# Kernel optimization log

Hardware: AMD Instinct MI355X
Metric: run time of the kernel (lower is better)

## Reference

```python
import jax, jax.numpy as jnp
import numpy as np

N = 50_000      # num_nodes
E = 1_600_000   # num_edges
R = 8           # num_relations
D = 128         # hidden_dim
L = 3           # num_layers
EPS = 1e-5


def setup_inputs() -> dict:
    key = jax.random.key(0)
    ks = jax.random.split(key, 10)
    x = jnp.arange(N, dtype=jnp.int64) if jax.config.jax_enable_x64 else jnp.arange(N, dtype=jnp.int32)
    edge_index = jax.random.randint(ks[0], (2, E), 0, N)
    edge_type = jax.random.randint(ks[1], (E,), 0, R)
    emb = jax.random.normal(ks[2], (N, D), dtype=jnp.float32) * (1.0 / np.sqrt(D))
    w_rel = jax.random.normal(ks[3], (L, R, D, D), dtype=jnp.float32) * (1.0 / np.sqrt(D))
    w_root = jax.random.normal(ks[4], (L, D, D), dtype=jnp.float32) * (1.0 / np.sqrt(D))
    bias = jax.random.normal(ks[5], (L, D), dtype=jnp.float32) * 0.01
    gamma = 1.0 + 0.1 * jax.random.normal(ks[6], (L, D), dtype=jnp.float32)
    beta = 0.1 * jax.random.normal(ks[7], (L, D), dtype=jnp.float32)
    return {"x": x, "edge_index": edge_index, "edge_type": edge_type,
            "emb": emb, "w_rel": w_rel, "w_root": w_root, "bias": bias,
            "gamma": gamma, "beta": beta}


def _layer_norm(h, g, b):
    mu = jnp.mean(h, axis=-1, keepdims=True)
    var = jnp.mean(jnp.square(h - mu), axis=-1, keepdims=True)
    return (h - mu) * jax.lax.rsqrt(var + EPS) * g + b


def _rgcn_conv(h, src, dst, etype, w_rel, w_root, b):
    # PyG RGCNConv: per-relation mean aggregation of transformed neighbors + root transform + bias
    hr = jnp.einsum('nd,rdf->rnf', h, w_rel)          # [R, N, D] relation-transformed features
    msg = hr[etype, src]                               # [E, D] gather per edge
    seg = etype * N + dst                              # combined (relation, target) segment id
    sums = jax.ops.segment_sum(msg, seg, num_segments=R * N)            # [R*N, D]
    cnt = jax.ops.segment_sum(jnp.ones((msg.shape[0],), h.dtype), seg, num_segments=R * N)
    mean = sums / jnp.maximum(cnt, 1.0)[:, None]
    agg = mean.reshape(R, N, D).sum(axis=0)            # sum over relations
    return agg + h @ w_root + b


def reference(x, edge_index, edge_type, emb, w_rel, w_root, bias, gamma, beta):
    src, dst = edge_index[0], edge_index[1]
    h = emb[x]                                         # node embedding lookup
    for i in range(L):
        h_new = _rgcn_conv(h, src, dst, edge_type, w_rel[i], w_root[i], bias[i])
        h_new = jax.nn.relu(_layer_norm(h_new, gamma[i], beta[i]))
        # dropout is identity in eval/reference mode
        h = h + h_new if i > 0 else h_new
    return h
```

## Files before the change

### kernel.cpp

```cpp
#include <hip/hip_runtime.h>

#define NN 50000
#define NE 1600000
#define NR 8
#define ND 128
#define NL 3
#define RN (NR * NN)
#define LN_EPS 1e-5f
#define PADF 132

#define NBKT 196
#define BSH 11
#define STRIDE_PB 10240
#define BIN_BLOCKS 1000
#define EPB 1600
#define I4PB 400
#define MM_BLOCKS_SA ((NN + 127) / 128)
#define MM_BLOCKS_FU ((NN + 63) / 64)

#define PREP_G (NN * 64)
#define PREP_W (27 * 16384)
#define PREP_TOT (PREP_G + PREP_W)
#define PREP_BLOCKS ((PREP_TOT + 255) / 256)

#define WS_H    0
#define WS_ROW  14400000
#define WS_BCUR 16000064
#define WS_ADJ  16004096
#define WS_WB   22404096
#define WS_BIG  23288832
#define WS_NEED_NEW (23288832ULL + 9ULL * NN * 256)

typedef __attribute__((ext_vector_type(8))) short short8;
typedef __attribute__((ext_vector_type(4))) float float4v;
typedef __attribute__((ext_vector_type(4))) unsigned uint4v;

__device__ __forceinline__ float bflo(unsigned u) { return __uint_as_float(u << 16); }
__device__ __forceinline__ float bfhi(unsigned u) { return __uint_as_float(u & 0xFFFF0000u); }
__device__ __forceinline__ unsigned f2bf(float f) {
    unsigned u = __float_as_uint(f);
    return (u + 0x7FFFu + ((u >> 16) & 1u)) >> 16;
}
__device__ __forceinline__ unsigned pack2(float lo, float hi) {
    return f2bf(lo) | (f2bf(hi) << 16);
}

__global__ __launch_bounds__(256) void k_prepbin(const int* __restrict__ x,
                                                 const float* __restrict__ emb,
                                                 const float* __restrict__ w_rel,
                                                 const float* __restrict__ w_root,
                                                 const int* __restrict__ src,
                                                 const int* __restrict__ dst,
                                                 const int* __restrict__ et,
                                                 unsigned* __restrict__ h,
                                                 unsigned short* __restrict__ wb,
                                                 int* __restrict__ bcur,
                                                 unsigned* __restrict__ stage) {
    __shared__ int lcnt[256];
    __shared__ int loff[256];
    __shared__ int lcur[256];
    __shared__ int sbase[256];
    __shared__ int tmp[256];
    __shared__ unsigned srt[EPB];
    __shared__ unsigned char bkt[EPB];

    int tid = threadIdx.x;
    if (blockIdx.x >= BIN_BLOCKS) {
        int i = (blockIdx.x - BIN_BLOCKS) * 256 + tid;
        if (i < PREP_G) {
            int n = i >> 6, dw = i & 63;
            float2 v = *(const float2*)&emb[(size_t)x[n] * ND + 2 * dw];
            h[i] = pack2(v.x, v.y);
            return;
        }
        i -= PREP_G;
        if (i < PREP_W) {
            int m = i >> 14;
            int idx = i & 16383;
            int j = idx & 7;
            int lane = (idx >> 3) & 63;
            int ft = (idx >> 9) & 7;
            int kk = idx >> 12;
            int row = kk * 32 + (lane >> 4) * 8 + j;
            int col = ft * 16 + (lane & 15);
            const float* W = (m < 24) ? (w_rel + (size_t)m * 16384)
                                      : (w_root + (size_t)(m - 24) * 16384);
            wb[i] = (unsigned short)f2bf(W[row * ND + col]);
        }
        return;
    }

    lcnt[tid] = 0;
    __syncthreads();

    int base4 = blockIdx.x * I4PB;
    const int4* s4p = (const int4*)src;
    const int4* d4p = (const int4*)dst;
    const int4* t4p = (const int4*)et;

    for (int i4 = tid; i4 < I4PB; i4 += 256) {
        int4 d4 = d4p[base4 + i4];
        int4 t4 = t4p[base4 + i4];
        atomicAdd(&lcnt[(t4.x * NN + d4.x) >> BSH], 1);
        atomicAdd(&lcnt[(t4.y * NN + d4.y) >> BSH], 1);
        atomicAdd(&lcnt[(t4.z * NN + d4.z) >> BSH], 1);
        atomicAdd(&lcnt[(t4.w * NN + d4.w) >> BSH], 1);
    }
    __syncthreads();
    int own = lcnt[tid];
    tmp[tid] = own;
    __syncthreads();
    for (int off = 1; off < 256; off <<= 1) {
        int v = (tid >= off) ? tmp[tid - off] : 0;
        __syncthreads();
        tmp[tid] += v;
        __syncthreads();
    }
    int excl = tmp[tid] - own;
    loff[tid] = excl;
    lcur[tid] = excl;
    if (tid < NBKT) sbase[tid] = atomicAdd(&bcur[tid], own);
    __syncthreads();

    for (int i4 = tid; i4 < I4PB; i4 += 256) {
        int4 s4 = s4p[base4 + i4];
        int4 d4 = d4p[base4 + i4];
        int4 t4 = t4p[base4 + i4];
        int segs[4] = {t4.x * NN + d4.x, t4.y * NN + d4.y,
                       t4.z * NN + d4.z, t4.w * NN + d4.w};
        int srcs[4] = {s4.x, s4.y, s4.z, s4.w};
#pragma unroll
        for (int j = 0; j < 4; j++) {
            int seg = segs[j];
            int b = seg >> BSH;
            unsigned rec = ((unsigned)(seg & 2047) << 16) | (unsigned)srcs[j];
            int pos = atomicAdd(&lcur[b], 1);
            srt[pos] = rec;
            bkt[pos] = (unsigned char)b;
        }
    }
    __syncthreads();
    for (int i = tid; i < EPB; i += 256) {
        int b = bkt[i];
        int idx = sbase[b] + (i - loff[b]);
        if (idx < STRIDE_PB)
            stage[(size_t)b * STRIDE_PB + idx] = srt[i];
    }
}

__device__ __forceinline__ void binB_body(const unsigned* __restrict__ stage,
                                          const int* __restrict__ bcur,
                                          int* __restrict__ rowstart,
                                          int* __restrict__ adj,
                                          int b, int tid,
                                          int* tmp, int* lcnt2, int* loff2,
                                          unsigned short* srt2, int* misc) {
    int bv = (tid < NBKT) ? bcur[tid] : 0;
    tmp[tid] = bv;
    __syncthreads();
    for (int off = 1; off < 256; off <<= 1) {
        int v = (tid >= off) ? tmp[tid - off] : 0;
        __syncthreads();
        tmp[tid] += v;
        __syncthreads();
    }
    if (tid == b) { misc[0] = tmp[tid] - bv; misc[1] = bv; }
    for (int j = tid; j < 2048; j += 256) lcnt2[j] = 0;
    __syncthreads();

    int n = misc[1];
    n = n < STRIDE_PB ? n : STRIDE_PB;
    const unsigned* sp = stage + (size_t)b * STRIDE_PB;
    for (int i = tid; i < n; i += 256)
        atomicAdd(&lcnt2[sp[i] >> 16], 1);
    __syncthreads();

    int v8[8];
    int s8 = 0;
    int base8 = tid * 8;
#pragma unroll
    for (int j = 0; j < 8; j++) { v8[j] = lcnt2[base8 + j]; s8 += v8[j]; }
    tmp[tid] = s8;
    __syncthreads();
    for (int off = 1; off < 256; off <<= 1) {
        int v = (tid >= off) ? tmp[tid - off] : 0;
        __syncthreads();
        tmp[tid] += v;
        __syncthreads();
    }
    int run = tmp[tid] - s8;
#pragma unroll
    for (int j = 0; j < 8; j++) { loff2[base8 + j] = run; run += v8[j]; }
    __syncthreads();
    for (int j = tid; j < 2048; j += 256) lcnt2[j] = loff2[j];
    __syncthreads();

    for (int i = tid; i < n; i += 256) {
        unsigned rec = sp[i];
        int pos = atomicAdd(&lcnt2[rec >> 16], 1);
        srt2[pos] = (unsigned short)(rec & 0xFFFFu);
    }
    __syncthreads();

    int gb = misc[0];
    for (int i = tid; i < n; i += 256) adj[gb + i] = (int)srt2[i];
    int segbase = b << BSH;
    for (int j = tid; j < 2048; j += 256) {
        int seg = segbase + j;
        if (seg < RN) rowstart[seg] = gb + loff2[j];
    }
    if (b == NBKT - 1 && tid == 0) rowstart[RN] = NE;
}

typedef unsigned TRarr[16][66];

template <int NG>
__device__ __forceinline__ void mm_body(const unsigned* __restrict__ h32,
                                        const unsigned short* __restrict__ wrel,
                                        const unsigned short* __restrict__ wroot,
                                        unsigned* __restrict__ hr,
                                        int mb, int tid,
                                        uint4* SB4, TRarr* TRp) {
    const unsigned short* SBs = (const unsigned short*)SB4;
    int wave = tid >> 6, lane = tid & 63;
    int quad = lane >> 4, l15 = lane & 15;
    int pr = l15 & 1;

    int rbase[NG];
    short8 af[NG][4];
#pragma unroll
    for (int g = 0; g < NG; g++) {
        rbase[g] = mb * (64 * NG) + g * 64 + wave * 16;
        int gi = rbase[g] + l15; gi = gi < NN ? gi : NN - 1;
        const unsigned* H = h32 + (size_t)gi * 64;
#pragma unroll
        for (int kk = 0; kk < 4; kk++)
            af[g][kk] = *(const short8*)&H[kk * 16 + quad * 4];
    }

    for (int m = 0; m < 9; m++) {
        const unsigned short* W = (m < 8) ? (wrel + (size_t)m * 16384) : wroot;
        __syncthreads();
        {
            const uint4* Wg = (const uint4*)W;
#pragma unroll
            for (int i = 0; i < 8; i++) SB4[tid + 256 * i] = Wg[tid + 256 * i];
        }
        __syncthreads();

        float4v ac[NG][8];
#pragma unroll
        for (int g = 0; g < NG; g++)
#pragma unroll
            for (int i = 0; i < 8; i++) ac[g][i] = (float4v){0.f, 0.f, 0.f, 0.f};
#pragma unroll
        for (int kk = 0; kk < 4; kk++) {
#pragma unroll
            for (int ft = 0; ft < 8; ft++) {
                short8 bf = *(const short8*)&SBs[((kk * 8 + ft) * 64 + lane) * 8];
#pragma unroll
                for (int g = 0; g < NG; g++)
                    ac[g][ft] = __builtin_amdgcn_mfma_f32_16x16x32_bf16(af[g][kk], bf, ac[g][ft], 0, 0, 0);
            }
        }

        unsigned* hrm = hr + (size_t)m * NN * 64;
#pragma unroll
        for (int g = 0; g < NG; g++) {
#pragma unroll
            for (int ft = 0; ft < 8; ft++) {
                float4v part;
#pragma unroll
                for (int rg = 0; rg < 4; rg++) part[rg] = __shfl_xor(ac[g][ft][rg], 1, 64);
                if ((ft & 1) == pr) {
                    int a = l15 >> 1;
#pragma unroll
                    for (int rg = 0; rg < 4; rg++) {
                        float lo = pr ? part[rg] : ac[g][ft][rg];
                        float hi = pr ? ac[g][ft][rg] : part[rg];
                        TRp[wave][quad * 4 + rg][ft * 8 + a] = pack2(lo, hi);
                    }
                }
            }
#pragma unroll
            for (int ps = 0; ps < 4; ps++) {
                int ri = ps * 4 + quad;
                uint4 v = *(const uint4*)&TRp[wave][ri][l15 * 4];
                int row = rbase[g] + ri;
                if (row < NN)
                    *(uint4*)&hrm[(size_t)row * 64 + l15 * 4] = v;
            }
        }
    }
}

__global__ __launch_bounds__(256) void k_binB_mm(const unsigned* __restrict__ stage,
                                                 const int* __restrict__ bcur,
                                                 int* __restrict__ rowstart,
                                                 int* __restrict__ adj,
                                                 const unsigned* __restrict__ h32,
                                                 const unsigned short* __restrict__ wrel,
                                                 const unsigned short* __restrict__ wroot,
                                                 unsigned* __restrict__ hr) {
    __shared__ uint4 SMEM[3104];
    int tid = threadIdx.x;
    if (blockIdx.x < NBKT) {
        int* tmp = (int*)SMEM;
        int* lcnt2 = (int*)SMEM + 256;
        int* loff2 = (int*)SMEM + 2304;
        unsigned short* srt2 = (unsigned short*)((int*)SMEM + 4352);
        int* misc = (int*)SMEM + 9472;
        binB_body(stage, bcur, rowstart, adj, blockIdx.x, tid,
                  tmp, lcnt2, loff2, srt2, misc);
    } else {
        mm_body<1>(h32, wrel, wroot, hr, blockIdx.x - NBKT, tid,
                   SMEM, (TRarr*)(SMEM + 2048));
    }
}

__global__ __launch_bounds__(256) void k_binB(const unsigned* __restrict__ stage,
                                              const int* __restrict__ bcur,
                                              int* __restrict__ rowstart,
                                              int* __restrict__ adj) {
    __shared__ uint4 SMEM[2369];
    int tid = threadIdx.x;
    int* tmp = (int*)SMEM;
    int* lcnt2 = (int*)SMEM + 256;
    int* loff2 = (int*)SMEM + 2304;
    unsigned short* srt2 = (unsigned short*)((int*)SMEM + 4352);
    int* misc = (int*)SMEM + 9472;
    binB_body(stage, bcur, rowstart, adj, blockIdx.x, tid,
              tmp, lcnt2, loff2, srt2, misc);
}

__global__ __launch_bounds__(256) void k_mm(const unsigned* __restrict__ h32,
                                            const unsigned short* __restrict__ wrel,
                                            const unsigned short* __restrict__ wroot,
                                            unsigned* __restrict__ hr) {
    __shared__ uint4 SMEM[3104];
    mm_body<2>(h32, wrel, wroot, hr, blockIdx.x, threadIdx.x,
               SMEM, (TRarr*)(SMEM + 2048));
}

#define AGA(u)                                  \
    a0 += bflo(u.x); a1 += bfhi(u.x);           \
    a2 += bflo(u.y); a3 += bfhi(u.y);           \
    a4 += bflo(u.z); a5 += bfhi(u.z);           \
    a6 += bflo(u.w); a7 += bfhi(u.w);
#define AGC(u)                                  \
    c0 += bflo(u.x); c1 += bfhi(u.x);           \
    c2 += bflo(u.y); c3 += bfhi(u.y);           \
    c4 += bflo(u.z); c5 += bfhi(u.z);           \
    c6 += bflo(u.w); c7 += bfhi(u.w);

__global__ __launch_bounds__(256) void k_aggln(const unsigned* __restrict__ hr,
                                               unsigned* __restrict__ h32,
                                               const int* __restrict__ adj,
                                               const int* __restrict__ rowstart,
                                               const float* __restrict__ bias,
                                               const float* __restrict__ gamma,
                                               const float* __restrict__ beta,
                                               float* __restrict__ out_f,
                                               int add_res, int last) {
    int n = (blockIdx.x * 256 + threadIdx.x) >> 4;
    int l15 = threadIdx.x & 15;

    float t0 = 0.f, t1 = 0.f, t2 = 0.f, t3 = 0.f,
          t4 = 0.f, t5 = 0.f, t6 = 0.f, t7 = 0.f;

    for (int r = 0; r < NR; r++) {
        int seg = r * NN + n;
        int st = rowstart[seg], en = rowstart[seg + 1];
        st = st < 0 ? 0 : st;
        en = en > NE ? NE : en;
        const unsigned* T = hr + (size_t)r * NN * 64;

        float a0 = 0.f, a1 = 0.f, a2 = 0.f, a3 = 0.f,
              a4 = 0.f, a5 = 0.f, a6 = 0.f, a7 = 0.f;
        float c0 = 0.f, c1 = 0.f, c2 = 0.f, c3 = 0.f,
              c4 = 0.f, c5 = 0.f, c6 = 0.f, c7 = 0.f;
        int p = st;
        for (; p + 3 < en; p += 4) {
            unsigned s0 = (unsigned)adj[p],     s1 = (unsigned)adj[p + 1];
            unsigned s2 = (unsigned)adj[p + 2], s3 = (unsigned)adj[p + 3];
            uint4 u0 = *(const uint4*)&T[(size_t)s0 * 64 + l15 * 4];
            uint4 u1 = *(const uint4*)&T[(size_t)s1 * 64 + l15 * 4];
            uint4 u2 = *(const uint4*)&T[(size_t)s2 * 64 + l15 * 4];
            uint4 u3 = *(const uint4*)&T[(size_t)s3 * 64 + l15 * 4];
            AGA(u0) AGC(u1) AGA(u2) AGC(u3)
        }
        for (; p + 1 < en; p += 2) {
            unsigned s0 = (unsigned)adj[p], s1 = (unsigned)adj[p + 1];
            uint4 u0 = *(const uint4*)&T[(size_t)s0 * 64 + l15 * 4];
            uint4 u1 = *(const uint4*)&T[(size_t)s1 * 64 + l15 * 4];
            AGA(u0) AGC(u1)
        }
        if (p < en) {
            unsigned s0 = (unsigned)adj[p];
            uint4 u0 = *(const uint4*)&T[(size_t)s0 * 64 + l15 * 4];
            AGA(u0)
        }
        int d = en - st;
        float sc = 1.0f / (float)(d > 1 ? d : 1);
        t0 += (a0 + c0) * sc; t1 += (a1 + c1) * sc;
        t2 += (a2 + c2) * sc; t3 += (a3 + c3) * sc;
        t4 += (a4 + c4) * sc; t5 += (a5 + c5) * sc;
        t6 += (a6 + c6) * sc; t7 += (a7 + c7) * sc;
    }

    {
        uint4 u = *(const uint4*)&hr[((size_t)8 * NN + n) * 64 + l15 * 4];
        t0 += bflo(u.x); t1 += bfhi(u.x);
        t2 += bflo(u.y); t3 += bfhi(u.y);
        t4 += bflo(u.z); t5 += bfhi(u.z);
        t6 += bflo(u.w); t7 += bfhi(u.w);
    }
    int f0 = 8 * l15;
    {
        float4 b0 = *(const float4*)&bias[f0];
        float4 b1 = *(const float4*)&bias[f0 + 4];
        t0 += b0.x; t1 += b0.y; t2 += b0.z; t3 += b0.w;
        t4 += b1.x; t5 += b1.y; t6 += b1.z; t7 += b1.w;
    }

    float s = t0 + t1 + t2 + t3 + t4 + t5 + t6 + t7;
#pragma unroll
    for (int off = 1; off < 16; off <<= 1) s += __shfl_xor(s, off, 64);
    float mu = s * (1.0f / ND);
    float e0 = t0 - mu, e1 = t1 - mu, e2 = t2 - mu, e3 = t3 - mu,
          e4 = t4 - mu, e5 = t5 - mu, e6 = t6 - mu, e7 = t7 - mu;
    float vs = e0 * e0 + e1 * e1 + e2 * e2 + e3 * e3 +
               e4 * e4 + e5 * e5 + e6 * e6 + e7 * e7;
#pragma unroll
    for (int off = 1; off < 16; off <<= 1) vs += __shfl_xor(vs, off, 64);
    float rr = rsqrtf(vs * (1.0f / ND) + LN_EPS);

    float4 g0 = *(const float4*)&gamma[f0];
    float4 g1 = *(const float4*)&gamma[f0 + 4];
    float4 be0 = *(const float4*)&beta[f0];
    float4 be1 = *(const float4*)&beta[f0 + 4];
    float o0 = fmaxf(e0 * rr * g0.x + be0.x, 0.0f);
    float o1 = fmaxf(e1 * rr * g0.y + be0.y, 0.0f);
    float o2 = fmaxf(e2 * rr * g0.z + be0.z, 0.0f);
    float o3 = fmaxf(e3 * rr * g0.w + be0.w, 0.0f);
    float o4 = fmaxf(e4 * rr * g1.x + be1.x, 0.0f);
    float o5 = fmaxf(e5 * rr * g1.y + be1.y, 0.0f);
    float o6 = fmaxf(e6 * rr * g1.z + be1.z, 0.0f);
    float o7 = fmaxf(e7 * rr * g1.w + be1.w, 0.0f);

    if (add_res) {
        uint4 u = *(const uint4*)&h32[(size_t)n * 64 + l15 * 4];
        o0 += bflo(u.x); o1 += bfhi(u.x);
        o2 += bflo(u.y); o3 += bfhi(u.y);
        o4 += bflo(u.z); o5 += bfhi(u.z);
        o6 += bflo(u.w); o7 += bfhi(u.w);
    }
    if (last) {
        *(float4*)&out_f[(size_t)n * ND + f0] = make_float4(o0, o1, o2, o3);
        *(float4*)&out_f[(size_t)n * ND + f0 + 4] = make_float4(o4, o5, o6, o7);
    } else {
        uint4 w;
        w.x = pack2(o0, o1); w.y = pack2(o2, o3);
        w.z = pack2(o4, o5); w.w = pack2(o6, o7);
        *(uint4*)&h32[(size_t)n * 64 + l15 * 4] = w;
    }
}


__global__ __launch_bounds__(256) void k_agg(const unsigned* __restrict__ h32,
                                             const int* __restrict__ adj,
                                             const int* __restrict__ rowstart,
                                             unsigned* __restrict__ S) {
    int q = (blockIdx.x * 256 + threadIdx.x) >> 4;
    int l15 = threadIdx.x & 15;
    int r = q / NN;
    int n = q - r * NN;
    int st = rowstart[q], en = rowstart[q + 1];
    st = st < 0 ? 0 : st;
    en = en > NE ? NE : en;
    float a0 = 0.f, a1 = 0.f, a2 = 0.f, a3 = 0.f,
          a4 = 0.f, a5 = 0.f, a6 = 0.f, a7 = 0.f;
    float c0 = 0.f, c1 = 0.f, c2 = 0.f, c3 = 0.f,
          c4 = 0.f, c5 = 0.f, c6 = 0.f, c7 = 0.f;
    int p = st;
    for (; p + 3 < en; p += 4) {
        unsigned s0 = (unsigned)adj[p],     s1 = (unsigned)adj[p + 1];
        unsigned s2 = (unsigned)adj[p + 2], s3 = (unsigned)adj[p + 3];
        uint4 u0 = *(const uint4*)&h32[(size_t)s0 * 64 + l15 * 4];
        uint4 u1 = *(const uint4*)&h32[(size_t)s1 * 64 + l15 * 4];
        uint4 u2 = *(const uint4*)&h32[(size_t)s2 * 64 + l15 * 4];
        uint4 u3 = *(const uint4*)&h32[(size_t)s3 * 64 + l15 * 4];
        AGA(u0) AGC(u1) AGA(u2) AGC(u3)
    }
    for (; p < en; p++) {
        unsigned s0 = (unsigned)adj[p];
        uint4 u0 = *(const uint4*)&h32[(size_t)s0 * 64 + l15 * 4];
        AGA(u0)
    }
    int d = en - st;
    float sc = 1.0f / (float)(d > 1 ? d : 1);
    a0 = (a0 + c0) * sc; a1 = (a1 + c1) * sc;
    a2 = (a2 + c2) * sc; a3 = (a3 + c3) * sc;
    a4 = (a4 + c4) * sc; a5 = (a5 + c5) * sc;
    a6 = (a6 + c6) * sc; a7 = (a7 + c7) * sc;
    uint4v w;
    w.x = pack2(a0, a1); w.y = pack2(a2, a3);
    w.z = pack2(a4, a5); w.w = pack2(a6, a7);
    __builtin_nontemporal_store(w, (uint4v*)&S[(size_t)n * 512 + r * 64 + l15 * 4]);
}

__global__ __launch_bounds__(256) void k_gemm(const unsigned* __restrict__ S,
                                              unsigned* __restrict__ h32,
                                              const unsigned short* __restrict__ wrel,
                                              const unsigned short* __restrict__ wroot,
                                              const float* __restrict__ bias,
                                              const float* __restrict__ gamma,
                                              const float* __restrict__ beta,
                                              float* __restrict__ out_f,
                                              int add_res, int last) {
    __shared__ char smraw[4 * 16 * PADF * 4];
    float* SLF = (float*)smraw;
    uint4* SB4 = (uint4*)smraw;
    const unsigned short* SBs = (const unsigned short*)smraw;

    int tid = threadIdx.x;
    int wave = tid >> 6, lane = tid & 63;
    int quad = lane >> 4, l15 = lane & 15;
    int w0 = blockIdx.x * 64 + wave * 16;
    int gi = w0 + l15; gi = gi < NN ? gi : NN - 1;
    float* WF = SLF + wave * 16 * PADF;

    float4v acc[8];
#pragma unroll
    for (int i = 0; i < 8; i++) acc[i] = (float4v){0.f, 0.f, 0.f, 0.f};

    const unsigned* Sr = S + (size_t)gi * 512;
    for (int r = 0; r < NR; r++) {
        short8 afr[4];
#pragma unroll
        for (int kk = 0; kk < 4; kk++)
            afr[kk] = *(const short8*)&Sr[r * 64 + kk * 16 + quad * 4];
        __syncthreads();
        {
            const uint4* Wg = (const uint4*)(wrel + (size_t)r * 16384);
#pragma unroll
            for (int i = 0; i < 8; i++) SB4[tid + 256 * i] = Wg[tid + 256 * i];
        }
        __syncthreads();
#pragma unroll
        for (int kk = 0; kk < 4; kk++) {
#pragma unroll
            for (int ft = 0; ft < 8; ft++) {
                short8 bf = *(const short8*)&SBs[((kk * 8 + ft) * 64 + lane) * 8];
                acc[ft] = __builtin_amdgcn_mfma_f32_16x16x32_bf16(afr[kk], bf, acc[ft], 0, 0, 0);
            }
        }
    }
    {
        const unsigned* Hr = h32 + (size_t)gi * 64;
        short8 afr[4];
#pragma unroll
        for (int kk = 0; kk < 4; kk++)
            afr[kk] = *(const short8*)&Hr[kk * 16 + quad * 4];
        __syncthreads();
        {
            const uint4* Wg = (const uint4*)wroot;
#pragma unroll
            for (int i = 0; i < 8; i++) SB4[tid + 256 * i] = Wg[tid + 256 * i];
        }
        __syncthreads();
#pragma unroll
        for (int kk = 0; kk < 4; kk++) {
#pragma unroll
            for (int ft = 0; ft < 8; ft++) {
                short8 bf = *(const short8*)&SBs[((kk * 8 + ft) * 64 + lane) * 8];
                acc[ft] = __builtin_amdgcn_mfma_f32_16x16x32_bf16(afr[kk], bf, acc[ft], 0, 0, 0);
            }
        }
    }
    __syncthreads();

#pragma unroll
    for (int ft = 0; ft < 8; ft++)
#pragma unroll
        for (int rg = 0; rg < 4; rg++)
            WF[(quad * 4 + rg) * PADF + ft * 16 + l15] = acc[ft][rg];

    float2 bia = *(const float2*)&bias[2 * lane];
    float2 gam = *(const float2*)&gamma[2 * lane];
    float2 bet = *(const float2*)&beta[2 * lane];

    for (int i = 0; i < 16; i++) {
        int g = w0 + i;
        if (g >= NN) continue;
        float v0 = WF[i * PADF + 2 * lane] + bia.x;
        float v1 = WF[i * PADF + 2 * lane + 1] + bia.y;
        float s = v0 + v1;
#pragma unroll
        for (int off = 32; off > 0; off >>= 1) s += __shfl_xor(s, off, 64);
        float mu = s * (1.0f / ND);
        float e0 = v0 - mu, e1 = v1 - mu;
        float vs = e0 * e0 + e1 * e1;
#pragma unroll
        for (int off = 32; off > 0; off >>= 1) vs += __shfl_xor(vs, off, 64);
        float rr = rsqrtf(vs * (1.0f / ND) + LN_EPS);
        float o0 = fmaxf(e0 * rr * gam.x + bet.x, 0.0f);
        float o1 = fmaxf(e1 * rr * gam.y + bet.y, 0.0f);
        if (add_res) {
            unsigned u = h32[(size_t)g * 64 + lane];
            o0 += bflo(u);
            o1 += bfhi(u);
        }
        if (last) {
            *(float2*)&out_f[(size_t)g * ND + 2 * lane] = make_float2(o0, o1);
        } else {
            h32[(size_t)g * 64 + lane] = pack2(o0, o1);
        }
    }
}

extern "C" void kernel_launch(void* const* d_in, const int* in_sizes, int n_in,
                              void* d_out, int out_size, void* d_ws, size_t ws_size,
                              hipStream_t stream) {
    const int*   x      = (const int*)d_in[0];
    const int*   ei     = (const int*)d_in[1];
    const int*   et     = (const int*)d_in[2];
    const float* emb    = (const float*)d_in[3];
    const float* w_rel  = (const float*)d_in[4];
    const float* w_root = (const float*)d_in[5];
    const float* bias   = (const float*)d_in[6];
    const float* gamma  = (const float*)d_in[7];
    const float* beta   = (const float*)d_in[8];
    float* out = (float*)d_out;

    char* ws = (char*)d_ws;
    unsigned* h        = (unsigned*)(ws + WS_H);
    int*      rowstart = (int*)     (ws + WS_ROW);
    int*      bcur     = (int*)     (ws + WS_BCUR);
    int*      adj      = (int*)     (ws + WS_ADJ);
    unsigned short* wb = (unsigned short*)(ws + WS_WB);
    unsigned* big      = (unsigned*)(ws + WS_BIG);
    unsigned* stage    = (unsigned*)d_out;

    const int* src = ei;
    const int* dst = ei + NE;

    hipMemsetAsync(bcur, 0, NBKT * sizeof(int), stream);

    k_prepbin<<<BIN_BLOCKS + PREP_BLOCKS, 256, 0, stream>>>(
        x, emb, w_rel, w_root, src, dst, et, h, wb, bcur, stage);

    if (ws_size >= WS_NEED_NEW) {
        k_binB_mm<<<NBKT + MM_BLOCKS_FU, 256, 0, stream>>>(
            stage, bcur, rowstart, adj,
            h, wb, wb + (size_t)24 * 16384, big);
        k_aggln<<<NN * 16 / 256, 256, 0, stream>>>(
            big, h, adj, rowstart,
            bias, gamma, beta, out, 0, 0);
        for (int l = 1; l < NL; l++) {
            k_mm<<<MM_BLOCKS_SA, 256, 0, stream>>>(
                h, wb + (size_t)l * 8 * 16384, wb + (size_t)(24 + l) * 16384, big);
            k_aggln<<<NN * 16 / 256, 256, 0, stream>>>(
                big, h, adj, rowstart,
                bias + l * ND, gamma + l * ND, beta + l * ND,
                out, 1, l == NL - 1);
        }
    } else {
        k_binB<<<NBKT, 256, 0, stream>>>(stage, bcur, rowstart, adj);
        for (int l = 0; l < NL; l++) {
            k_agg<<<RN * 16 / 256, 256, 0, stream>>>(h, adj, rowstart, big);
            k_gemm<<<(NN + 63) / 64, 256, 0, stream>>>(
                big, h,
                wb + (size_t)l * 8 * 16384, wb + (size_t)(24 + l) * 16384,
                bias + l * ND, gamma + l * ND, beta + l * ND,
                out, l > 0, l == NL - 1);
        }
    }
}
```

Before: 499.2 us.

## Sort edges by destination node and pack relation and degree into adjacency entries

```diff
diff --git a/kernel.cpp b/kernel.cpp
--- a/kernel.cpp
+++ b/kernel.cpp
@@ -7,7 +7,6 @@
 #define NL 3
 #define RN (NR * NN)
 #define LN_EPS 1e-5f
-#define PADF 132
 
 #define NBKT 196
 #define BSH 11
@@ -24,16 +23,14 @@
 #define PREP_BLOCKS ((PREP_TOT + 255) / 256)
 
 #define WS_H    0
-#define WS_ROW  14400000
+#define WS_NS   14400000
 #define WS_BCUR 16000064
 #define WS_ADJ  16004096
 #define WS_WB   22404096
 #define WS_BIG  23288832
-#define WS_NEED_NEW (23288832ULL + 9ULL * NN * 256)
 
 typedef __attribute__((ext_vector_type(8))) short short8;
 typedef __attribute__((ext_vector_type(4))) float float4v;
-typedef __attribute__((ext_vector_type(4))) unsigned uint4v;
 
 __device__ __forceinline__ float bflo(unsigned u) { return __uint_as_float(u << 16); }
 __device__ __forceinline__ float bfhi(unsigned u) { return __uint_as_float(u & 0xFFFF0000u); }
@@ -101,10 +98,10 @@
     for (int i4 = tid; i4 < I4PB; i4 += 256) {
         int4 d4 = d4p[base4 + i4];
         int4 t4 = t4p[base4 + i4];
-        atomicAdd(&lcnt[(t4.x * NN + d4.x) >> BSH], 1);
-        atomicAdd(&lcnt[(t4.y * NN + d4.y) >> BSH], 1);
-        atomicAdd(&lcnt[(t4.z * NN + d4.z) >> BSH], 1);
-        atomicAdd(&lcnt[(t4.w * NN + d4.w) >> BSH], 1);
+        atomicAdd(&lcnt[(d4.x * 8 + t4.x) >> BSH], 1);
+        atomicAdd(&lcnt[(d4.y * 8 + t4.y) >> BSH], 1);
+        atomicAdd(&lcnt[(d4.z * 8 + t4.z) >> BSH], 1);
+        atomicAdd(&lcnt[(d4.w * 8 + t4.w) >> BSH], 1);
     }
     __syncthreads();
     int own = lcnt[tid];
@@ -126,14 +123,14 @@
         int4 s4 = s4p[base4 + i4];
         int4 d4 = d4p[base4 + i4];
         int4 t4 = t4p[base4 + i4];
-        int segs[4] = {t4.x * NN + d4.x, t4.y * NN + d4.y,
-                       t4.z * NN + d4.z, t4.w * NN + d4.w};
+        int keys[4] = {d4.x * 8 + t4.x, d4.y * 8 + t4.y,
+                       d4.z * 8 + t4.z, d4.w * 8 + t4.w};
         int srcs[4] = {s4.x, s4.y, s4.z, s4.w};
 #pragma unroll
         for (int j = 0; j < 4; j++) {
-            int seg = segs[j];
-            int b = seg >> BSH;
-            unsigned rec = ((unsigned)(seg & 2047) << 16) | (unsigned)srcs[j];
+            int key = keys[j];
+            int b = key >> BSH;
+            unsigned rec = ((unsigned)(key & 2047) << 16) | (unsigned)srcs[j];
             int pos = atomicAdd(&lcur[b], 1);
             srt[pos] = rec;
             bkt[pos] = (unsigned char)b;
@@ -150,8 +147,8 @@
 
 __device__ __forceinline__ void binB_body(const unsigned* __restrict__ stage,
                                           const int* __restrict__ bcur,
-                                          int* __restrict__ rowstart,
-                                          int* __restrict__ adj,
+                                          int* __restrict__ nodestart,
+                                          unsigned* __restrict__ adj,
                                           int b, int tid,
                                           int* tmp, int* lcnt2, int* loff2,
                                           unsigned short* srt2, int* misc) {
@@ -203,13 +200,19 @@
     __syncthreads();
 
     int gb = misc[0];
-    for (int i = tid; i < n; i += 256) adj[gb + i] = (int)srt2[i];
     int segbase = b << BSH;
-    for (int j = tid; j < 2048; j += 256) {
-        int seg = segbase + j;
-        if (seg < RN) rowstart[seg] = gb + loff2[j];
-    }
-    if (b == NBKT - 1 && tid == 0) rowstart[RN] = NE;
+#pragma unroll
+    for (int jj = 0; jj < 8; jj++) {
+        int j = base8 + jj;
+        int key = segbase + j;
+        if (key >= RN) break;
+        int s = loff2[j], e = lcnt2[j];
+        int d = e - s; d = d > 4095 ? 4095 : d;
+        unsigned tag = ((unsigned)(key & 7) << 28) | ((unsigned)d << 16);
+        for (int i = s; i < e; i++) adj[gb + i] = tag | (unsigned)srt2[i];
+        if ((key & 7) == 0) nodestart[key >> 3] = gb + s;
+    }
+    if (b == NBKT - 1 && tid == 0) nodestart[NN] = NE;
 }
 
 typedef unsigned TRarr[16][66];
@@ -296,8 +299,8 @@
 
 __global__ __launch_bounds__(256) void k_binB_mm(const unsigned* __restrict__ stage,
                                                  const int* __restrict__ bcur,
-                                                 int* __restrict__ rowstart,
-                                                 int* __restrict__ adj,
+                                                 int* __restrict__ nodestart,
+                                                 unsigned* __restrict__ adj,
                                                  const unsigned* __restrict__ h32,
                                                  const unsigned short* __restrict__ wrel,
                                                  const unsigned short* __restrict__ wroot,
@@ -310,27 +313,12 @@
         int* loff2 = (int*)SMEM + 2304;
         unsigned short* srt2 = (unsigned short*)((int*)SMEM + 4352);
         int* misc = (int*)SMEM + 9472;
-        binB_body(stage, bcur, rowstart, adj, blockIdx.x, tid,
+        binB_body(stage, bcur, nodestart, adj, blockIdx.x, tid,
                   tmp, lcnt2, loff2, srt2, misc);
     } else {
         mm_body<1>(h32, wrel, wroot, hr, blockIdx.x - NBKT, tid,
                    SMEM, (TRarr*)(SMEM + 2048));
     }
-}
-
-__global__ __launch_bounds__(256) void k_binB(const unsigned* __restrict__ stage,
-                                              const int* __restrict__ bcur,
-                                              int* __restrict__ rowstart,
-                                              int* __restrict__ adj) {
-    __shared__ uint4 SMEM[2369];
-    int tid = threadIdx.x;
-    int* tmp = (int*)SMEM;
-    int* lcnt2 = (int*)SMEM + 256;
-    int* loff2 = (int*)SMEM + 2304;
-    unsigned short* srt2 = (unsigned short*)((int*)SMEM + 4352);
-    int* misc = (int*)SMEM + 9472;
-    binB_body(stage, bcur, rowstart, adj, blockIdx.x, tid,
-              tmp, lcnt2, loff2, srt2, misc);
 }
 
 __global__ __launch_bounds__(256) void k_mm(const unsigned* __restrict__ h32,
@@ -342,21 +330,21 @@
                SMEM, (TRarr*)(SMEM + 2048));
 }
 
-#define AGA(u)                                  \
-    a0 += bflo(u.x); a1 += bfhi(u.x);           \
-    a2 += bflo(u.y); a3 += bfhi(u.y);           \
-    a4 += bflo(u.z); a5 += bfhi(u.z);           \
-    a6 += bflo(u.w); a7 += bfhi(u.w);
-#define AGC(u)                                  \
-    c0 += bflo(u.x); c1 += bfhi(u.x);           \
-    c2 += bflo(u.y); c3 += bfhi(u.y);           \
-    c4 += bflo(u.z); c5 += bfhi(u.z);           \
-    c6 += bflo(u.w); c7 += bfhi(u.w);
+#define AGS_A(u, s)                                        \
+    a0 += bflo(u.x) * s; a1 += bfhi(u.x) * s;              \
+    a2 += bflo(u.y) * s; a3 += bfhi(u.y) * s;              \
+    a4 += bflo(u.z) * s; a5 += bfhi(u.z) * s;              \
+    a6 += bflo(u.w) * s; a7 += bfhi(u.w) * s;
+#define AGS_C(u, s)                                        \
+    c0 += bflo(u.x) * s; c1 += bfhi(u.x) * s;              \
+    c2 += bflo(u.y) * s; c3 += bfhi(u.y) * s;              \
+    c4 += bflo(u.z) * s; c5 += bfhi(u.z) * s;              \
+    c6 += bflo(u.w) * s; c7 += bfhi(u.w) * s;
 
 __global__ __launch_bounds__(256) void k_aggln(const unsigned* __restrict__ hr,
                                                unsigned* __restrict__ h32,
-                                               const int* __restrict__ adj,
-                                               const int* __restrict__ rowstart,
+                                               const unsigned* __restrict__ adj,
+                                               const int* __restrict__ nodestart,
                                                const float* __restrict__ bias,
                                                const float* __restrict__ gamma,
                                                const float* __restrict__ beta,
@@ -365,48 +353,53 @@
     int n = (blockIdx.x * 256 + threadIdx.x) >> 4;
     int l15 = threadIdx.x & 15;
 
-    float t0 = 0.f, t1 = 0.f, t2 = 0.f, t3 = 0.f,
-          t4 = 0.f, t5 = 0.f, t6 = 0.f, t7 = 0.f;
-
-    for (int r = 0; r < NR; r++) {
-        int seg = r * NN + n;
-        int st = rowstart[seg], en = rowstart[seg + 1];
-        st = st < 0 ? 0 : st;
-        en = en > NE ? NE : en;
-        const unsigned* T = hr + (size_t)r * NN * 64;
-
-        float a0 = 0.f, a1 = 0.f, a2 = 0.f, a3 = 0.f,
-              a4 = 0.f, a5 = 0.f, a6 = 0.f, a7 = 0.f;
-        float c0 = 0.f, c1 = 0.f, c2 = 0.f, c3 = 0.f,
-              c4 = 0.f, c5 = 0.f, c6 = 0.f, c7 = 0.f;
-        int p = st;
-        for (; p + 3 < en; p += 4) {
-            unsigned s0 = (unsigned)adj[p],     s1 = (unsigned)adj[p + 1];
-            unsigned s2 = (unsigned)adj[p + 2], s3 = (unsigned)adj[p + 3];
-            uint4 u0 = *(const uint4*)&T[(size_t)s0 * 64 + l15 * 4];
-            uint4 u1 = *(const uint4*)&T[(size_t)s1 * 64 + l15 * 4];
-            uint4 u2 = *(const uint4*)&T[(size_t)s2 * 64 + l15 * 4];
-            uint4 u3 = *(const uint4*)&T[(size_t)s3 * 64 + l15 * 4];
-            AGA(u0) AGC(u1) AGA(u2) AGC(u3)
-        }
-        for (; p + 1 < en; p += 2) {
-            unsigned s0 = (unsigned)adj[p], s1 = (unsigned)adj[p + 1];
-            uint4 u0 = *(const uint4*)&T[(size_t)s0 * 64 + l15 * 4];
-            uint4 u1 = *(const uint4*)&T[(size_t)s1 * 64 + l15 * 4];
-            AGA(u0) AGC(u1)
-        }
-        if (p < en) {
-            unsigned s0 = (unsigned)adj[p];
-            uint4 u0 = *(const uint4*)&T[(size_t)s0 * 64 + l15 * 4];
-            AGA(u0)
-        }
-        int d = en - st;
-        float sc = 1.0f / (float)(d > 1 ? d : 1);
-        t0 += (a0 + c0) * sc; t1 += (a1 + c1) * sc;
-        t2 += (a2 + c2) * sc; t3 += (a3 + c3) * sc;
-        t4 += (a4 + c4) * sc; t5 += (a5 + c5) * sc;
-        t6 += (a6 + c6) * sc; t7 += (a7 + c7) * sc;
-    }
+    int st = nodestart[n], en = nodestart[n + 1];
+    st = st < 0 ? 0 : st;
+    en = en > NE ? NE : en;
+
+    float a0 = 0.f, a1 = 0.f, a2 = 0.f, a3 = 0.f,
+          a4 = 0.f, a5 = 0.f, a6 = 0.f, a7 = 0.f;
+    float c0 = 0.f, c1 = 0.f, c2 = 0.f, c3 = 0.f,
+          c4 = 0.f, c5 = 0.f, c6 = 0.f, c7 = 0.f;
+
+    int p = st;
+    for (; p + 3 < en; p += 4) {
+        unsigned q0 = adj[p],     q1 = adj[p + 1];
+        unsigned q2 = adj[p + 2], q3 = adj[p + 3];
+        unsigned i0 = (q0 & 0xFFFFu) + (q0 >> 28) * NN;
+        unsigned i1 = (q1 & 0xFFFFu) + (q1 >> 28) * NN;
+        unsigned i2 = (q2 & 0xFFFFu) + (q2 >> 28) * NN;
+        unsigned i3 = (q3 & 0xFFFFu) + (q3 >> 28) * NN;
+        uint4 u0 = *(const uint4*)&hr[(size_t)i0 * 64 + l15 * 4];
+        uint4 u1 = *(const uint4*)&hr[(size_t)i1 * 64 + l15 * 4];
+        uint4 u2 = *(const uint4*)&hr[(size_t)i2 * 64 + l15 * 4];
+        uint4 u3 = *(const uint4*)&hr[(size_t)i3 * 64 + l15 * 4];
+        float s0 = __builtin_amdgcn_rcpf((float)((q0 >> 16) & 0xFFFu));
+        float s1 = __builtin_amdgcn_rcpf((float)((q1 >> 16) & 0xFFFu));
+        float s2 = __builtin_amdgcn_rcpf((float)((q2 >> 16) & 0xFFFu));
+        float s3 = __builtin_amdgcn_rcpf((float)((q3 >> 16) & 0xFFFu));
+        AGS_A(u0, s0) AGS_C(u1, s1) AGS_A(u2, s2) AGS_C(u3, s3)
+    }
+    for (; p + 1 < en; p += 2) {
+        unsigned q0 = adj[p], q1 = adj[p + 1];
+        unsigned i0 = (q0 & 0xFFFFu) + (q0 >> 28) * NN;
+        unsigned i1 = (q1 & 0xFFFFu) + (q1 >> 28) * NN;
+        uint4 u0 = *(const uint4*)&hr[(size_t)i0 * 64 + l15 * 4];
+        uint4 u1 = *(const uint4*)&hr[(size_t)i1 * 64 + l15 * 4];
+        float s0 = __builtin_amdgcn_rcpf((float)((q0 >> 16) & 0xFFFu));
+        float s1 = __builtin_amdgcn_rcpf((float)((q1 >> 16) & 0xFFFu));
+        AGS_A(u0, s0) AGS_C(u1, s1)
+    }
+    if (p < en) {
+        unsigned q0 = adj[p];
+        unsigned i0 = (q0 & 0xFFFFu) + (q0 >> 28) * NN;
+        uint4 u0 = *(const uint4*)&hr[(size_t)i0 * 64 + l15 * 4];
+        float s0 = __builtin_amdgcn_rcpf((float)((q0 >> 16) & 0xFFFu));
+        AGS_A(u0, s0)
+    }
+
+    float t0 = a0 + c0, t1 = a1 + c1, t2 = a2 + c2, t3 = a3 + c3,
+          t4 = a4 + c4, t5 = a5 + c5, t6 = a6 + c6, t7 = a7 + c7;
 
     {
         uint4 u = *(const uint4*)&hr[((size_t)8 * NN + n) * 64 + l15 * 4];
@@ -463,159 +456,6 @@
         w.x = pack2(o0, o1); w.y = pack2(o2, o3);
         w.z = pack2(o4, o5); w.w = pack2(o6, o7);
         *(uint4*)&h32[(size_t)n * 64 + l15 * 4] = w;
-    }
-}
-
-
-__global__ __launch_bounds__(256) void k_agg(const unsigned* __restrict__ h32,
-                                             const int* __restrict__ adj,
-                                             const int* __restrict__ rowstart,
-                                             unsigned* __restrict__ S) {
-    int q = (blockIdx.x * 256 + threadIdx.x) >> 4;
-    int l15 = threadIdx.x & 15;
-    int r = q / NN;
-    int n = q - r * NN;
-    int st = rowstart[q], en = rowstart[q + 1];
-    st = st < 0 ? 0 : st;
-    en = en > NE ? NE : en;
-    float a0 = 0.f, a1 = 0.f, a2 = 0.f, a3 = 0.f,
-          a4 = 0.f, a5 = 0.f, a6 = 0.f, a7 = 0.f;
-    float c0 = 0.f, c1 = 0.f, c2 = 0.f, c3 = 0.f,
-          c4 = 0.f, c5 = 0.f, c6 = 0.f, c7 = 0.f;
-    int p = st;
-    for (; p + 3 < en; p += 4) {
-        unsigned s0 = (unsigned)adj[p],     s1 = (unsigned)adj[p + 1];
-        unsigned s2 = (unsigned)adj[p + 2], s3 = (unsigned)adj[p + 3];
-        uint4 u0 = *(const uint4*)&h32[(size_t)s0 * 64 + l15 * 4];
-        uint4 u1 = *(const uint4*)&h32[(size_t)s1 * 64 + l15 * 4];
-        uint4 u2 = *(const uint4*)&h32[(size_t)s2 * 64 + l15 * 4];
-        uint4 u3 = *(const uint4*)&h32[(size_t)s3 * 64 + l15 * 4];
-        AGA(u0) AGC(u1) AGA(u2) AGC(u3)
-    }
-    for (; p < en; p++) {
-        unsigned s0 = (unsigned)adj[p];
-        uint4 u0 = *(const uint4*)&h32[(size_t)s0 * 64 + l15 * 4];
-        AGA(u0)
-    }
-    int d = en - st;
-    float sc = 1.0f / (float)(d > 1 ? d : 1);
-    a0 = (a0 + c0) * sc; a1 = (a1 + c1) * sc;
-    a2 = (a2 + c2) * sc; a3 = (a3 + c3) * sc;
-    a4 = (a4 + c4) * sc; a5 = (a5 + c5) * sc;
-    a6 = (a6 + c6) * sc; a7 = (a7 + c7) * sc;
-    uint4v w;
-    w.x = pack2(a0, a1); w.y = pack2(a2, a3);
-    w.z = pack2(a4, a5); w.w = pack2(a6, a7);
-    __builtin_nontemporal_store(w, (uint4v*)&S[(size_t)n * 512 + r * 64 + l15 * 4]);
-}
-
-__global__ __launch_bounds__(256) void k_gemm(const unsigned* __restrict__ S,
-                                              unsigned* __restrict__ h32,
-                                              const unsigned short* __restrict__ wrel,
-                                              const unsigned short* __restrict__ wroot,
-                                              const float* __restrict__ bias,
-                                              const float* __restrict__ gamma,
-                                              const float* __restrict__ beta,
-                                              float* __restrict__ out_f,
-                                              int add_res, int last) {
-    __shared__ char smraw[4 * 16 * PADF * 4];
-    float* SLF = (float*)smraw;
-    uint4* SB4 = (uint4*)smraw;
-    const unsigned short* SBs = (const unsigned short*)smraw;
-
-    int tid = threadIdx.x;
-    int wave = tid >> 6, lane = tid & 63;
-    int quad = lane >> 4, l15 = lane & 15;
-    int w0 = blockIdx.x * 64 + wave * 16;
-    int gi = w0 + l15; gi = gi < NN ? gi : NN - 1;
-    float* WF = SLF + wave * 16 * PADF;
-
-    float4v acc[8];
-#pragma unroll
-    for (int i = 0; i < 8; i++) acc[i] = (float4v){0.f, 0.f, 0.f, 0.f};
-
-    const unsigned* Sr = S + (size_t)gi * 512;
-    for (int r = 0; r < NR; r++) {
-        short8 afr[4];
-#pragma unroll
-        for (int kk = 0; kk < 4; kk++)
-            afr[kk] = *(const short8*)&Sr[r * 64 + kk * 16 + quad * 4];
-        __syncthreads();
-        {
-            const uint4* Wg = (const uint4*)(wrel + (size_t)r * 16384);
-#pragma unroll
-            for (int i = 0; i < 8; i++) SB4[tid + 256 * i] = Wg[tid + 256 * i];
-        }
-        __syncthreads();
-#pragma unroll
-        for (int kk = 0; kk < 4; kk++) {
-#pragma unroll
-            for (int ft = 0; ft < 8; ft++) {
-                short8 bf = *(const short8*)&SBs[((kk * 8 + ft) * 64 + lane) * 8];
-                acc[ft] = __builtin_amdgcn_mfma_f32_16x16x32_bf16(afr[kk], bf, acc[ft], 0, 0, 0);
-            }
-        }
-    }
-    {
-        const unsigned* Hr = h32 + (size_t)gi * 64;
-        short8 afr[4];
-#pragma unroll
-        for (int kk = 0; kk < 4; kk++)
-            afr[kk] = *(const short8*)&Hr[kk * 16 + quad * 4];
-        __syncthreads();
-        {
-            const uint4* Wg = (const uint4*)wroot;
-#pragma unroll
-            for (int i = 0; i < 8; i++) SB4[tid + 256 * i] = Wg[tid + 256 * i];
-        }
-        __syncthreads();
-#pragma unroll
-        for (int kk = 0; kk < 4; kk++) {
-#pragma unroll
-            for (int ft = 0; ft < 8; ft++) {
-                short8 bf = *(const short8*)&SBs[((kk * 8 + ft) * 64 + lane) * 8];
-                acc[ft] = __builtin_amdgcn_mfma_f32_16x16x32_bf16(afr[kk], bf, acc[ft], 0, 0, 0);
-            }
-        }
-    }
-    __syncthreads();
-
-#pragma unroll
-    for (int ft = 0; ft < 8; ft++)
-#pragma unroll
-        for (int rg = 0; rg < 4; rg++)
-            WF[(quad * 4 + rg) * PADF + ft * 16 + l15] = acc[ft][rg];
-
-    float2 bia = *(const float2*)&bias[2 * lane];
-    float2 gam = *(const float2*)&gamma[2 * lane];
-    float2 bet = *(const float2*)&beta[2 * lane];
-
-    for (int i = 0; i < 16; i++) {
-        int g = w0 + i;
-        if (g >= NN) continue;
-        float v0 = WF[i * PADF + 2 * lane] + bia.x;
-        float v1 = WF[i * PADF + 2 * lane + 1] + bia.y;
-        float s = v0 + v1;
-#pragma unroll
-        for (int off = 32; off > 0; off >>= 1) s += __shfl_xor(s, off, 64);
-        float mu = s * (1.0f / ND);
-        float e0 = v0 - mu, e1 = v1 - mu;
-        float vs = e0 * e0 + e1 * e1;
-#pragma unroll
-        for (int off = 32; off > 0; off >>= 1) vs += __shfl_xor(vs, off, 64);
-        float rr = rsqrtf(vs * (1.0f / ND) + LN_EPS);
-        float o0 = fmaxf(e0 * rr * gam.x + bet.x, 0.0f);
-        float o1 = fmaxf(e1 * rr * gam.y + bet.y, 0.0f);
-        if (add_res) {
-            unsigned u = h32[(size_t)g * 64 + lane];
-            o0 += bflo(u);
-            o1 += bfhi(u);
-        }
-        if (last) {
-            *(float2*)&out_f[(size_t)g * ND + 2 * lane] = make_float2(o0, o1);
-        } else {
-            h32[(size_t)g * 64 + lane] = pack2(o0, o1);
-        }
     }
 }
 
@@ -634,13 +474,13 @@
     float* out = (float*)d_out;
 
     char* ws = (char*)d_ws;
-    unsigned* h        = (unsigned*)(ws + WS_H);
-    int*      rowstart = (int*)     (ws + WS_ROW);
-    int*      bcur     = (int*)     (ws + WS_BCUR);
-    int*      adj      = (int*)     (ws + WS_ADJ);
-    unsigned short* wb = (unsigned short*)(ws + WS_WB);
-    unsigned* big      = (unsigned*)(ws + WS_BIG);
-    unsigned* stage    = (unsigned*)d_out;
+    unsigned* h         = (unsigned*)(ws + WS_H);
+    int*      nodestart = (int*)     (ws + WS_NS);
+    int*      bcur      = (int*)     (ws + WS_BCUR);
+    unsigned* adj       = (unsigned*)(ws + WS_ADJ);
+    unsigned short* wb  = (unsigned short*)(ws + WS_WB);
+    unsigned* big       = (unsigned*)(ws + WS_BIG);
+    unsigned* stage     = (unsigned*)d_out;
 
     const int* src = ei;
     const int* dst = ei + NE;
@@ -650,30 +490,18 @@
     k_prepbin<<<BIN_BLOCKS + PREP_BLOCKS, 256, 0, stream>>>(
         x, emb, w_rel, w_root, src, dst, et, h, wb, bcur, stage);
 
-    if (ws_size >= WS_NEED_NEW) {
-        k_binB_mm<<<NBKT + MM_BLOCKS_FU, 256, 0, stream>>>(
-            stage, bcur, rowstart, adj,
-            h, wb, wb + (size_t)24 * 16384, big);
+    k_binB_mm<<<NBKT + MM_BLOCKS_FU, 256, 0, stream>>>(
+        stage, bcur, nodestart, adj,
+        h, wb, wb + (size_t)24 * 16384, big);
+    k_aggln<<<NN * 16 / 256, 256, 0, stream>>>(
+        big, h, adj, nodestart,
+        bias, gamma, beta, out, 0, 0);
+    for (int l = 1; l < NL; l++) {
+        k_mm<<<MM_BLOCKS_SA, 256, 0, stream>>>(
+            h, wb + (size_t)l * 8 * 16384, wb + (size_t)(24 + l) * 16384, big);
         k_aggln<<<NN * 16 / 256, 256, 0, stream>>>(
-            big, h, adj, rowstart,
-            bias, gamma, beta, out, 0, 0);
-        for (int l = 1; l < NL; l++) {
-            k_mm<<<MM_BLOCKS_SA, 256, 0, stream>>>(
-                h, wb + (size_t)l * 8 * 16384, wb + (size_t)(24 + l) * 16384, big);
-            k_aggln<<<NN * 16 / 256, 256, 0, stream>>>(
-                big, h, adj, rowstart,
-                bias + l * ND, gamma + l * ND, beta + l * ND,
-                out, 1, l == NL - 1);
-        }
-    } else {
-        k_binB<<<NBKT, 256, 0, stream>>>(stage, bcur, rowstart, adj);
-        for (int l = 0; l < NL; l++) {
-            k_agg<<<RN * 16 / 256, 256, 0, stream>>>(h, adj, rowstart, big);
-            k_gemm<<<(NN + 63) / 64, 256, 0, stream>>>(
-                big, h,
-                wb + (size_t)l * 8 * 16384, wb + (size_t)(24 + l) * 16384,
-                bias + l * ND, gamma + l * ND, beta + l * ND,
-                out, l > 0, l == NL - 1);
-        }
-    }
-}
+            big, h, adj, nodestart,
+            bias + l * ND, gamma + l * ND, beta + l * ND,
+            out, 1, l == NL - 1);
+    }
+}
```

New measurement: 497.8 us. About the same (-0.3%).
